# Performance work log

Hardware: AMD Instinct MI355X
Metric: run time of the kernel (lower is better)

## Reference

```python
import jax, jax.numpy as jnp
import numpy as np
import math

EMBED_DIM = 1024
NUM_HEADS = 16
DEPTH = 12
HEAD_DIM = EMBED_DIM // NUM_HEADS // 2  # 32
LAMBDA_INIT = 0.8 - 0.6 * math.exp(-0.3 * DEPTH)
SCALE = HEAD_DIM ** -0.5  # flash_attn default softmax scale
RMS_EPS = 1e-5
BATCH, SEQ = 2, 2048


def _freqs(seq_len):
    # angle = 1 / 10000 ** linspace(0, 1, head_dim//2); freqs = pos * angle
    angle = 1.0 / 10000.0 ** jnp.linspace(0.0, 1.0, HEAD_DIM // 2)
    idx = jnp.arange(seq_len, dtype=jnp.float32)
    f = idx[:, None] * angle[None, :]
    return jnp.cos(f), jnp.sin(f)


def _rope_interleaved(x, cos, sin):
    # x: (b, t, h, d); cos/sin: (t, d//2). Interleaved pairs (0,1),(2,3),...
    x1, x2 = x[..., 0::2], x[..., 1::2]
    c = cos[None, :, None, :]
    s = sin[None, :, None, :]
    o1 = x1 * c - x2 * s
    o2 = x1 * s + x2 * c
    return jnp.stack([o1, o2], axis=-1).reshape(x.shape)


def _forward(x, Wq, Wk, Wv, Wo, lambda_q1, lambda_k1, lambda_q2, lambda_k2, rms_weight):
    b, t, _ = x.shape
    q = (x @ Wq.T).reshape(b, t, 2 * NUM_HEADS, HEAD_DIM)
    k = (x @ Wk.T).reshape(b, t, 2 * NUM_HEADS, HEAD_DIM)
    v = (x @ Wv.T).reshape(b, t, NUM_HEADS, 2, HEAD_DIM)
    cos, sin = _freqs(t)
    q = _rope_interleaved(q, cos, sin)
    k = _rope_interleaved(k, cos, sin)
    # split the 2H axis into (H, 2): q1/q2 are even/odd sub-heads
    q = q.reshape(b, t, NUM_HEADS, 2, HEAD_DIM)
    k = k.reshape(b, t, NUM_HEADS, 2, HEAD_DIM)
    q1, q2 = q[..., 0, :], q[..., 1, :]
    k1, k2 = k[..., 0, :], k[..., 1, :]
    v12 = v.reshape(b, t, NUM_HEADS, 2 * HEAD_DIM)  # == concat(v1, v2) on last dim

    def attend(qh, kh):
        scores = jnp.einsum('bthd,bshd->bhts', qh, kh) * SCALE
        p = jax.nn.softmax(scores, axis=-1)  # non-causal, as in source
        return jnp.einsum('bhts,bshe->bthe', p, v12)  # (b, t, H, 2*hd)

    attn1 = attend(q1, k1)
    attn2 = attend(q2, k2)
    lam = (jnp.exp(jnp.sum(lambda_q1 * lambda_k1))
           - jnp.exp(jnp.sum(lambda_q2 * lambda_k2)) + LAMBDA_INIT)
    a = attn1 - lam * attn2
    # RMSNorm over last dim (2*head_dim) with affine weight
    a = a * jax.lax.rsqrt(jnp.mean(a * a, axis=-1, keepdims=True) + RMS_EPS) * rms_weight
    a = a * (1.0 - LAMBDA_INIT)
    a = a.reshape(b, t, NUM_HEADS * 2 * HEAD_DIM)
    return a @ Wo.T


def setup_inputs() -> dict:
    key = jax.random.key(0)
    ks = jax.random.split(key, 9)
    std = EMBED_DIM ** -0.5
    return {
        'x': jax.random.normal(ks[0], (BATCH, SEQ, EMBED_DIM), jnp.float32),
        'Wq': jax.random.normal(ks[1], (EMBED_DIM, EMBED_DIM), jnp.float32) * std,
        'Wk': jax.random.normal(ks[2], (EMBED_DIM, EMBED_DIM), jnp.float32) * std,
        'Wv': jax.random.normal(ks[3], (EMBED_DIM, EMBED_DIM), jnp.float32) * std,
        'Wo': jax.random.normal(ks[4], (EMBED_DIM, EMBED_DIM), jnp.float32) * std,
        'lambda_q1': jax.random.normal(ks[5], (HEAD_DIM,), jnp.float32) * 0.1,
        'lambda_k1': jax.random.normal(ks[6], (HEAD_DIM,), jnp.float32) * 0.1,
        'lambda_q2': jax.random.normal(ks[7], (HEAD_DIM,), jnp.float32) * 0.1,
        'lambda_k2': jax.random.normal(ks[8], (HEAD_DIM,), jnp.float32) * 0.1,
        'rms_weight': jnp.ones((2 * HEAD_DIM,), jnp.float32),
    }


def reference(x, Wq, Wk, Wv, Wo, lambda_q1, lambda_k1, lambda_q2, lambda_k2, rms_weight):
    return _forward(x, Wq, Wk, Wv, Wo, lambda_q1, lambda_k1, lambda_q2, lambda_k2, rms_weight)
```

## Files before the change

kernel.cpp:

```cpp
#include <hip/hip_runtime.h>
#include <stdint.h>

typedef unsigned short u16;
typedef __bf16 bf16x8 __attribute__((ext_vector_type(8)));
typedef float f32x4 __attribute__((ext_vector_type(4)));
typedef float f32x16 __attribute__((ext_vector_type(16)));

#define TOKENS 4096
#define SEQLEN 2048
#define EMB 1024
#define NHEADS 16

static constexpr float LAMBDA_INIT_F = 0.7836057665316245f;
static constexpr float ONE_MINUS_LI  = 0.21639423346837553f;
static constexpr float SCALE_F       = 0.17677669529663687f;
static constexpr float LOG2E_F       = 1.4426950408889634f;

__device__ __forceinline__ u16 f2bf(float f) {
  uint32_t u = __builtin_bit_cast(uint32_t, f);
  u += 0x7fffu + ((u >> 16) & 1u);
  return (u16)(u >> 16);
}
__device__ __forceinline__ float bf2f(u16 h) {
  uint32_t u = ((uint32_t)h) << 16;
  return __builtin_bit_cast(float, u);
}
__device__ __forceinline__ float fast_exp2(float x) {
#if __has_builtin(__builtin_amdgcn_exp2f)
  return __builtin_amdgcn_exp2f(x);
#else
  return exp2f(x);
#endif
}
__device__ __forceinline__ void async16(const void* g, void* l) {
  __builtin_amdgcn_global_load_lds((__attribute__((address_space(1))) void*)(g),
                                   (__attribute__((address_space(3))) void*)(l),
                                   16, 0, 0);
}
__device__ __forceinline__ f32x4 mfma16(uint4 a, uint4 b, f32x4 c) {
  return __builtin_amdgcn_mfma_f32_16x16x32_bf16(
      __builtin_bit_cast(bf16x8, a), __builtin_bit_cast(bf16x8, b), c, 0, 0, 0);
}
__device__ __forceinline__ f32x16 mfma32(uint4 a, uint4 b, f32x16 c) {
  return __builtin_amdgcn_mfma_f32_32x32x16_bf16(
      __builtin_bit_cast(bf16x8, a), __builtin_bit_cast(bf16x8, b), c, 0, 0, 0);
}

__global__ __launch_bounds__(256) void prep_kernel(
    const float* __restrict__ x,  const float* __restrict__ wq,
    const float* __restrict__ wk, const float* __restrict__ wv,
    const float* __restrict__ wo, const float* __restrict__ lq1,
    const float* __restrict__ lk1,const float* __restrict__ lq2,
    const float* __restrict__ lk2,
    u16* __restrict__ xb, u16* __restrict__ wqb, u16* __restrict__ wkb,
    u16* __restrict__ wvb, u16* __restrict__ wob, float* __restrict__ lam_out)
{
  int i0 = (blockIdx.x * 256 + threadIdx.x) * 4;
  const float* src; u16* dst; int j;
  if (i0 < 4194304)      { src = x;  dst = xb;  j = i0; }
  else if (i0 < 5242880) { src = wq; dst = wqb; j = i0 - 4194304; }
  else if (i0 < 6291456) { src = wk; dst = wkb; j = i0 - 5242880; }
  else if (i0 < 7340032) { src = wv; dst = wvb; j = i0 - 6291456; }
  else                   { src = wo; dst = wob; j = i0 - 7340032; }
  float4 v = *(const float4*)(src + j);
  uint2 pack;
  pack.x = (uint32_t)f2bf(v.x) | ((uint32_t)f2bf(v.y) << 16);
  pack.y = (uint32_t)f2bf(v.z) | ((uint32_t)f2bf(v.w) << 16);
  *(uint2*)(dst + j) = pack;

  if (blockIdx.x == 0 && threadIdx.x == 0) {
    float d1 = 0.f, d2 = 0.f;
    for (int i = 0; i < 32; ++i) { d1 += lq1[i] * lk1[i]; d2 += lq2[i] * lk2[i]; }
    *lam_out = expf(d1) - expf(d2) + LAMBDA_INIT_F;
  }
}

template <int MODE>
__device__ __forceinline__ void gemm_body(const u16* __restrict__ A,
                                          const u16* __restrict__ B,
                                          void* __restrict__ C)
{
  __shared__ u16 As[128 * 64];
  __shared__ u16 Bs[128 * 64];
  const int t = threadIdx.x;
  const int lane = t & 63, w = t >> 6;
  const int q4 = lane >> 4, lm = lane & 15;
  const int wr = w >> 1, wc = w & 1;
  const int bm = blockIdx.y * 128, bn = blockIdx.x * 128;

  f32x4 acc[4][4];
#pragma unroll
  for (int mi = 0; mi < 4; ++mi)
#pragma unroll
    for (int ni = 0; ni < 4; ++ni) acc[mi][ni] = (f32x4){0.f, 0.f, 0.f, 0.f};

  for (int kt = 0; kt < 16; ++kt) {
    const int k0 = kt * 64;
    __syncthreads();
#pragma unroll
    for (int ro = 0; ro < 4; ++ro) {
      int ft = ro * 256 + t;
      int row = ft >> 3;
      int col = (((ft & 7) ^ (row & 7)) << 3);
      async16(&A[(bm + row) * 1024 + k0 + col], &As[ft * 8]);
      async16(&B[(bn + row) * 1024 + k0 + col], &Bs[ft * 8]);
    }
    __syncthreads();
#pragma unroll
    for (int ks = 0; ks < 2; ++ks) {
      uint4 af[4], bf[4];
#pragma unroll
      for (int mi = 0; mi < 4; ++mi)
        af[mi] = *(const uint4*)&As[(wr * 64 + mi * 16 + lm) * 64 +
                                    (((ks * 4 + q4) ^ (lm & 7)) << 3)];
#pragma unroll
      for (int ni = 0; ni < 4; ++ni)
        bf[ni] = *(const uint4*)&Bs[(wc * 64 + ni * 16 + lm) * 64 +
                                    (((ks * 4 + q4) ^ (lm & 7)) << 3)];
#pragma unroll
      for (int mi = 0; mi < 4; ++mi)
#pragma unroll
        for (int ni = 0; ni < 4; ++ni)
          acc[mi][ni] = mfma16(af[mi], bf[ni], acc[mi][ni]);
    }
  }
#pragma unroll
  for (int mi = 0; mi < 4; ++mi)
#pragma unroll
    for (int ni = 0; ni < 4; ++ni) {
      if (MODE == 2) {
        int token0 = bm + wr * 64 + mi * 16 + q4 * 4;
        int col = bn + wc * 64 + ni * 16 + lm;
        int bb = token0 >> 11, key0 = token0 & 2047;
        int h = col >> 6, d = col & 63;
        ushort4 pk;
        pk.x = f2bf(acc[mi][ni][0]);
        pk.y = f2bf(acc[mi][ni][1]);
        pk.z = f2bf(acc[mi][ni][2]);
        pk.w = f2bf(acc[mi][ni][3]);
        *(ushort4*)((u16*)C + ((size_t)((bb * 16 + h) * 64 + d)) * 2048 + key0) = pk;
      } else {
#pragma unroll
        for (int r = 0; r < 4; ++r) {
          int row = bm + wr * 64 + mi * 16 + q4 * 4 + r;
          int col = bn + wc * 64 + ni * 16 + lm;
          if (MODE == 1) ((float*)C)[row * 1024 + col] = acc[mi][ni][r];
          else           ((u16*)C)[row * 1024 + col]   = f2bf(acc[mi][ni][r]);
        }
      }
    }
}

__global__ __launch_bounds__(256) void gemm_qkv_kernel(
    const u16* __restrict__ xb, const u16* __restrict__ wqb,
    const u16* __restrict__ wkb, const u16* __restrict__ wvb,
    u16* __restrict__ qb, u16* __restrict__ kb, u16* __restrict__ vtb)
{
  if (blockIdx.z == 0)      gemm_body<0>(xb, wqb, qb);
  else if (blockIdx.z == 1) gemm_body<0>(xb, wkb, kb);
  else                      gemm_body<2>(xb, wvb, vtb);
}

__global__ __launch_bounds__(256) void gemm_out_kernel(
    const u16* __restrict__ ab, const u16* __restrict__ wob,
    float* __restrict__ out)
{
  gemm_body<1>(ab, wob, out);
}

__global__ __launch_bounds__(256) void rope_kernel(u16* __restrict__ qb,
                                                   u16* __restrict__ kb)
{
  int p = blockIdx.x * 256 + threadIdx.x;
  int tok = p >> 9;
  int pc = p & 511;
  int j = pc & 15;
  int tpos = tok & (SEQLEN - 1);
  float ang = exp2f(-(float)j * 0.8858474919699633f);
  float f = (float)tpos * ang;
  float s, c;
  sincosf(f, &s, &c);
  u16* ptr = ((blockIdx.y == 0) ? qb : kb) + tok * 1024 + pc * 2;
  uint32_t u = *(const uint32_t*)ptr;
  float x1 = bf2f((u16)(u & 0xffff));
  float x2 = bf2f((u16)(u >> 16));
  float o1 = x1 * c - x2 * s;
  float o2 = x1 * s + x2 * c;
  if (blockIdx.y == 0) { o1 *= SCALE_F * LOG2E_F; o2 *= SCALE_F * LOG2E_F; }
  *(uint32_t*)ptr = (uint32_t)f2bf(o1) | ((uint32_t)f2bf(o2) << 16);
}

__global__ __launch_bounds__(256) void attn_kernel(
    const u16* __restrict__ qb, const u16* __restrict__ kb,
    const u16* __restrict__ vtb, const float* __restrict__ lam_p,
    const float* __restrict__ rmsw, u16* __restrict__ ab)
{
  __shared__ u16 smem[16384];

  const int t = threadIdx.x;
  const int lane = t & 63, w = t >> 6;
  const int l5 = lane >> 5, lr = lane & 31;
  const int qt = blockIdx.x, h = blockIdx.y, b = blockIdx.z;
  const int tok0 = b * SEQLEN + qt * 128;
  const int hch = h * 64;

  const u16* kbase = kb + (size_t)(b * SEQLEN) * 1024 + hch;
  const u16* vbase = vtb + (size_t)((b * 16 + h) * 64) * 2048;
  u16* P = &smem[8192 + w * 2048];

#pragma unroll
  for (int ro = 0; ro < 4; ++ro) {
    int ft = ro * 256 + t;
    int row = ft >> 3;
    int col = (((ft & 7) ^ (row & 7)) << 3);
    async16(&qb[(tok0 + row) * 1024 + hch + col], &smem[8192 + ft * 8]);
  }
  __syncthreads();
  uint4 qf[2][2];
#pragma unroll
  for (int c = 0; c < 2; ++c)
#pragma unroll
    for (int kk = 0; kk < 2; ++kk)
      qf[c][kk] = *(const uint4*)&smem[8192 + (w * 32 + lr) * 64 +
                                       (((c * 4 + kk * 2 + l5) ^ (lr & 7)) << 3)];

  f32x16 O[2][2];
#pragma unroll
  for (int c = 0; c < 2; ++c)
#pragma unroll
    for (int n = 0; n < 2; ++n)
#pragma unroll
      for (int i = 0; i < 16; ++i) O[c][n][i] = 0.f;
  float rs[2] = {0.f, 0.f};
  uint4 vf[2][4];

  for (int kv = 0; kv < SEQLEN; kv += 64) {
    __syncthreads();
#pragma unroll
    for (int ro = 0; ro < 2; ++ro) {
      int ft = ro * 256 + t;
      int row = ft >> 3;
      int col = (((ft & 7) ^ (row & 7)) << 3);
      async16(kbase + (kv + row) * 1024 + col, &smem[ft * 8]);
      async16(vbase + row * 2048 + kv + col, &smem[4096 + ft * 8]);
    }
    __syncthreads();

#pragma unroll
    for (int c = 0; c < 2; ++c) {
#pragma unroll
      for (int kb2 = 0; kb2 < 2; ++kb2) {
        f32x16 s;
#pragma unroll
        for (int i = 0; i < 16; ++i) s[i] = 0.f;
#pragma unroll
        for (int kk = 0; kk < 2; ++kk) {
          uint4 kf = *(const uint4*)&smem[(kb2 * 32 + lr) * 64 +
                                          (((c * 4 + kk * 2 + l5) ^ (lr & 7)) << 3)];
          s = mfma32(kf, qf[c][kk], s);
        }
        float rloc = 0.f;
#pragma unroll
        for (int g = 0; g < 4; ++g) {
          float e0 = fast_exp2(s[g * 4 + 0]);
          float e1 = fast_exp2(s[g * 4 + 1]);
          float e2 = fast_exp2(s[g * 4 + 2]);
          float e3 = fast_exp2(s[g * 4 + 3]);
          rloc += (e0 + e1) + (e2 + e3);
          uint2 pk;
          pk.x = __builtin_amdgcn_perm(__builtin_bit_cast(uint32_t, e1),
                                       __builtin_bit_cast(uint32_t, e0), 0x07060302u);
          pk.y = __builtin_amdgcn_perm(__builtin_bit_cast(uint32_t, e3),
                                       __builtin_bit_cast(uint32_t, e2), 0x07060302u);
          *(uint2*)&P[lr * 64 + ((((kb2 * 4 + g) ^ (lr & 7)) << 3) + l5 * 4)] = pk;
        }
        rs[c] += rloc;
      }
      if (c == 0) {
#pragma unroll
        for (int n = 0; n < 2; ++n)
#pragma unroll
          for (int kc = 0; kc < 4; ++kc)
            vf[n][kc] = *(const uint4*)&smem[4096 + (n * 32 + lr) * 64 +
                                             (((kc * 2 + l5) ^ (lr & 7)) << 3)];
      }
#pragma unroll
      for (int kc = 0; kc < 4; ++kc) {
        uint4 af = *(const uint4*)&P[lr * 64 + (((kc * 2 + l5) ^ (lr & 7)) << 3)];
        O[c][0] = mfma32(af, vf[0][kc], O[c][0]);
        O[c][1] = mfma32(af, vf[1][kc], O[c][1]);
      }
    }
  }

  float lam = *lam_p;
  rs[0] += __shfl_xor(rs[0], 32);
  rs[1] += __shfl_xor(rs[1], 32);
  float inv1 = 1.f / rs[0];
  float inv2 = lam / rs[1];
  float wv2[2] = { rmsw[lr], rmsw[32 + lr] };
#pragma unroll
  for (int g = 0; g < 4; ++g) {
#pragma unroll
    for (int rr = 0; rr < 4; ++rr) {
      int r = g * 4 + rr;
      int qrl = rr + 8 * g + 4 * l5;
      float i1 = __shfl(inv1, qrl);
      float i2 = __shfl(inv2, qrl);
      float a0 = O[0][0][r] * i1 - O[1][0][r] * i2;
      float a1 = O[0][1][r] * i1 - O[1][1][r] * i2;
      float ssq = a0 * a0 + a1 * a1;
#pragma unroll
      for (int off = 16; off > 0; off >>= 1) ssq += __shfl_xor(ssq, off);
      float sc = rsqrtf(ssq * (1.f / 64.f) + 1e-5f) * ONE_MINUS_LI;
      int row = tok0 + w * 32 + qrl;
      ab[row * 1024 + hch + lr]      = f2bf(a0 * sc * wv2[0]);
      ab[row * 1024 + hch + 32 + lr] = f2bf(a1 * sc * wv2[1]);
    }
  }
}

extern "C" void kernel_launch(void* const* d_in, const int* in_sizes, int n_in,
                              void* d_out, int out_size, void* d_ws, size_t ws_size,
                              hipStream_t stream)
{
  (void)in_sizes; (void)n_in; (void)out_size; (void)ws_size;
  const float* x    = (const float*)d_in[0];
  const float* Wq   = (const float*)d_in[1];
  const float* Wk   = (const float*)d_in[2];
  const float* Wv   = (const float*)d_in[3];
  const float* Wo   = (const float*)d_in[4];
  const float* lq1  = (const float*)d_in[5];
  const float* lk1  = (const float*)d_in[6];
  const float* lq2  = (const float*)d_in[7];
  const float* lk2  = (const float*)d_in[8];
  const float* rmsw = (const float*)d_in[9];
  float* out = (float*)d_out;

  char* ws = (char*)d_ws;
  u16* xb   = (u16*)(ws + 0);
  u16* wqb  = (u16*)(ws + 8388608);
  u16* wkb  = (u16*)(ws + 10485760);
  u16* wvb  = (u16*)(ws + 12582912);
  u16* wob  = (u16*)(ws + 14680064);
  u16* qb   = (u16*)(ws + 16777216);
  u16* kb   = (u16*)(ws + 25165824);
  u16* vtb  = (u16*)(ws + 33554432);
  u16* ab   = (u16*)(ws + 41943040);
  float* lam = (float*)(ws + 50331648);

  hipLaunchKernelGGL(prep_kernel, dim3(8192), dim3(256), 0, stream,
                     x, Wq, Wk, Wv, Wo, lq1, lk1, lq2, lk2,
                     xb, wqb, wkb, wvb, wob, lam);
  hipLaunchKernelGGL(gemm_qkv_kernel, dim3(8, 32, 3), dim3(256), 0, stream,
                     xb, wqb, wkb, wvb, qb, kb, vtb);
  hipLaunchKernelGGL(rope_kernel, dim3(8192, 2), dim3(256), 0, stream, qb, kb);
  hipLaunchKernelGGL(attn_kernel, dim3(16, 16, 2), dim3(256), 0, stream,
                     qb, kb, vtb, lam, rmsw, ab);
  hipLaunchKernelGGL(gemm_out_kernel, dim3(8, 32, 1), dim3(256), 0, stream,
                     ab, wob, out);
}
```

Measured before the change: 252.8 us.

## Split attention sub-heads across waves and keep P in registers via lane shuffles

The attention kernel now uses 64-query tiles and twice as many blocks. Each wave handles one sub-head (c) for one 32-row group, instead of one wave handling both sub-heads for 32 rows. The P matrix is no longer round-tripped through shared memory: the S^T layout is computed and swapped between half-waves with shuffles to form the MFMA B operand directly. The differential combine now goes through shared memory between wave pairs. Shared memory is halved and launch bounds request 4 blocks per CU, which aims for better occupancy and less LDS traffic, at the cost of extra K/V tile loads per query and an extra sync and exchange in the epilogue.

```diff
diff --git a/kernel.cpp b/kernel.cpp
--- a/kernel.cpp
+++ b/kernel.cpp
@@ -190,49 +190,45 @@
   *(uint32_t*)ptr = (uint32_t)f2bf(o1) | ((uint32_t)f2bf(o2) << 16);
 }
 
-__global__ __launch_bounds__(256) void attn_kernel(
+__global__ __launch_bounds__(256, 4) void attn_kernel(
     const u16* __restrict__ qb, const u16* __restrict__ kb,
     const u16* __restrict__ vtb, const float* __restrict__ lam_p,
     const float* __restrict__ rmsw, u16* __restrict__ ab)
 {
-  __shared__ u16 smem[16384];
+  __shared__ u16 smem[8192];
 
   const int t = threadIdx.x;
   const int lane = t & 63, w = t >> 6;
   const int l5 = lane >> 5, lr = lane & 31;
+  const int c = w >> 1, rg = w & 1;
+  const bool hi = (l5 != 0);
   const int qt = blockIdx.x, h = blockIdx.y, b = blockIdx.z;
-  const int tok0 = b * SEQLEN + qt * 128;
+  const int tok0 = b * SEQLEN + qt * 64;
   const int hch = h * 64;
 
   const u16* kbase = kb + (size_t)(b * SEQLEN) * 1024 + hch;
   const u16* vbase = vtb + (size_t)((b * 16 + h) * 64) * 2048;
-  u16* P = &smem[8192 + w * 2048];
-
-#pragma unroll
-  for (int ro = 0; ro < 4; ++ro) {
+
+#pragma unroll
+  for (int ro = 0; ro < 2; ++ro) {
     int ft = ro * 256 + t;
     int row = ft >> 3;
     int col = (((ft & 7) ^ (row & 7)) << 3);
-    async16(&qb[(tok0 + row) * 1024 + hch + col], &smem[8192 + ft * 8]);
+    async16(&qb[(tok0 + row) * 1024 + hch + col], &smem[ft * 8]);
   }
   __syncthreads();
-  uint4 qf[2][2];
-#pragma unroll
-  for (int c = 0; c < 2; ++c)
-#pragma unroll
-    for (int kk = 0; kk < 2; ++kk)
-      qf[c][kk] = *(const uint4*)&smem[8192 + (w * 32 + lr) * 64 +
-                                       (((c * 4 + kk * 2 + l5) ^ (lr & 7)) << 3)];
-
-  f32x16 O[2][2];
-#pragma unroll
-  for (int c = 0; c < 2; ++c)
-#pragma unroll
-    for (int n = 0; n < 2; ++n)
-#pragma unroll
-      for (int i = 0; i < 16; ++i) O[c][n][i] = 0.f;
-  float rs[2] = {0.f, 0.f};
-  uint4 vf[2][4];
+  uint4 qf[2];
+#pragma unroll
+  for (int kk = 0; kk < 2; ++kk)
+    qf[kk] = *(const uint4*)&smem[(rg * 32 + lr) * 64 +
+                                  (((c * 4 + kk * 2 + l5) ^ (lr & 7)) << 3)];
+
+  f32x16 O[2];
+#pragma unroll
+  for (int db = 0; db < 2; ++db)
+#pragma unroll
+    for (int i = 0; i < 16; ++i) O[db][i] = 0.f;
+  float rs = 0.f;
 
   for (int kv = 0; kv < SEQLEN; kv += 64) {
     __syncthreads();
@@ -246,77 +242,117 @@
     }
     __syncthreads();
 
-#pragma unroll
-    for (int c = 0; c < 2; ++c) {
-#pragma unroll
-      for (int kb2 = 0; kb2 < 2; ++kb2) {
-        f32x16 s;
-#pragma unroll
-        for (int i = 0; i < 16; ++i) s[i] = 0.f;
-#pragma unroll
-        for (int kk = 0; kk < 2; ++kk) {
-          uint4 kf = *(const uint4*)&smem[(kb2 * 32 + lr) * 64 +
-                                          (((c * 4 + kk * 2 + l5) ^ (lr & 7)) << 3)];
-          s = mfma32(kf, qf[c][kk], s);
-        }
-        float rloc = 0.f;
-#pragma unroll
-        for (int g = 0; g < 4; ++g) {
-          float e0 = fast_exp2(s[g * 4 + 0]);
-          float e1 = fast_exp2(s[g * 4 + 1]);
-          float e2 = fast_exp2(s[g * 4 + 2]);
-          float e3 = fast_exp2(s[g * 4 + 3]);
-          rloc += (e0 + e1) + (e2 + e3);
-          uint2 pk;
-          pk.x = __builtin_amdgcn_perm(__builtin_bit_cast(uint32_t, e1),
-                                       __builtin_bit_cast(uint32_t, e0), 0x07060302u);
-          pk.y = __builtin_amdgcn_perm(__builtin_bit_cast(uint32_t, e3),
-                                       __builtin_bit_cast(uint32_t, e2), 0x07060302u);
-          *(uint2*)&P[lr * 64 + ((((kb2 * 4 + g) ^ (lr & 7)) << 3) + l5 * 4)] = pk;
-        }
-        rs[c] += rloc;
-      }
-      if (c == 0) {
-#pragma unroll
-        for (int n = 0; n < 2; ++n)
-#pragma unroll
-          for (int kc = 0; kc < 4; ++kc)
-            vf[n][kc] = *(const uint4*)&smem[4096 + (n * 32 + lr) * 64 +
-                                             (((kc * 2 + l5) ^ (lr & 7)) << 3)];
-      }
-#pragma unroll
-      for (int kc = 0; kc < 4; ++kc) {
-        uint4 af = *(const uint4*)&P[lr * 64 + (((kc * 2 + l5) ^ (lr & 7)) << 3)];
-        O[c][0] = mfma32(af, vf[0][kc], O[c][0]);
-        O[c][1] = mfma32(af, vf[1][kc], O[c][1]);
-      }
-    }
-  }
-
-  float lam = *lam_p;
-  rs[0] += __shfl_xor(rs[0], 32);
-  rs[1] += __shfl_xor(rs[1], 32);
-  float inv1 = 1.f / rs[0];
-  float inv2 = lam / rs[1];
-  float wv2[2] = { rmsw[lr], rmsw[32 + lr] };
-#pragma unroll
-  for (int g = 0; g < 4; ++g) {
-#pragma unroll
-    for (int rr = 0; rr < 4; ++rr) {
-      int r = g * 4 + rr;
-      int qrl = rr + 8 * g + 4 * l5;
-      float i1 = __shfl(inv1, qrl);
-      float i2 = __shfl(inv2, qrl);
-      float a0 = O[0][0][r] * i1 - O[1][0][r] * i2;
-      float a1 = O[0][1][r] * i1 - O[1][1][r] * i2;
-      float ssq = a0 * a0 + a1 * a1;
-#pragma unroll
-      for (int off = 16; off > 0; off >>= 1) ssq += __shfl_xor(ssq, off);
-      float sc = rsqrtf(ssq * (1.f / 64.f) + 1e-5f) * ONE_MINUS_LI;
-      int row = tok0 + w * 32 + qrl;
-      ab[row * 1024 + hch + lr]      = f2bf(a0 * sc * wv2[0]);
-      ab[row * 1024 + hch + 32 + lr] = f2bf(a1 * sc * wv2[1]);
-    }
+    uint4 vf[2][4];
+#pragma unroll
+    for (int db = 0; db < 2; ++db)
+#pragma unroll
+      for (int kc = 0; kc < 4; ++kc)
+        vf[db][kc] = *(const uint4*)&smem[4096 + (db * 32 + lr) * 64 +
+                                          (((kc * 2 + l5) ^ (lr & 7)) << 3)];
+
+#pragma unroll
+    for (int kb2 = 0; kb2 < 2; ++kb2) {
+      f32x16 s;
+#pragma unroll
+      for (int i = 0; i < 16; ++i) s[i] = 0.f;
+#pragma unroll
+      for (int kk = 0; kk < 2; ++kk) {
+        uint4 kf = *(const uint4*)&smem[(kb2 * 32 + lr) * 64 +
+                                        (((c * 4 + kk * 2 + l5) ^ (lr & 7)) << 3)];
+        s = mfma32(kf, qf[kk], s);
+      }
+      uint32_t pk[8];
+      float rloc = 0.f;
+#pragma unroll
+      for (int g = 0; g < 4; ++g) {
+        float e0 = fast_exp2(s[g * 4 + 0]);
+        float e1 = fast_exp2(s[g * 4 + 1]);
+        float e2 = fast_exp2(s[g * 4 + 2]);
+        float e3 = fast_exp2(s[g * 4 + 3]);
+        rloc += (e0 + e1) + (e2 + e3);
+        pk[2 * g]     = __builtin_amdgcn_perm(__builtin_bit_cast(uint32_t, e1),
+                                              __builtin_bit_cast(uint32_t, e0),
+                                              0x07060302u);
+        pk[2 * g + 1] = __builtin_amdgcn_perm(__builtin_bit_cast(uint32_t, e3),
+                                              __builtin_bit_cast(uint32_t, e2),
+                                              0x07060302u);
+      }
+      rs += rloc;
+#pragma unroll
+      for (int t2 = 0; t2 < 2; ++t2) {
+        uint32_t s0 = hi ? pk[4 * t2]     : pk[4 * t2 + 2];
+        uint32_t s1 = hi ? pk[4 * t2 + 1] : pk[4 * t2 + 3];
+        uint32_t r0 = (uint32_t)__shfl_xor((int)s0, 32);
+        uint32_t r1 = (uint32_t)__shfl_xor((int)s1, 32);
+        uint4 bfr;
+        bfr.x = hi ? r0 : pk[4 * t2];
+        bfr.y = hi ? r1 : pk[4 * t2 + 1];
+        bfr.z = hi ? pk[4 * t2 + 2] : r0;
+        bfr.w = hi ? pk[4 * t2 + 3] : r1;
+        O[0] = mfma32(vf[0][kb2 * 2 + t2], bfr, O[0]);
+        O[1] = mfma32(vf[1][kb2 * 2 + t2], bfr, O[1]);
+      }
+    }
+  }
+
+  rs += __shfl_xor(rs, 32);
+  const int row64 = rg * 32 + lr;
+  float* ex = (float*)smem;
+  __syncthreads();
+
+  if (c == 1) {
+    float inv2 = (*lam_p) / rs;
+#pragma unroll
+    for (int db = 0; db < 2; ++db)
+#pragma unroll
+      for (int g = 0; g < 4; ++g) {
+        int d0 = db * 32 + 8 * g + 4 * l5;
+        int ch = (d0 >> 2) ^ (lr & 7);
+        float4 v;
+        v.x = O[db][4 * g + 0] * inv2;
+        v.y = O[db][4 * g + 1] * inv2;
+        v.z = O[db][4 * g + 2] * inv2;
+        v.w = O[db][4 * g + 3] * inv2;
+        *(float4*)&ex[row64 * 64 + ch * 4] = v;
+      }
+  }
+  __syncthreads();
+  if (c == 0) {
+    float inv1 = 1.f / rs;
+    float4 a4[8];
+    float ssq = 0.f;
+#pragma unroll
+    for (int db = 0; db < 2; ++db)
+#pragma unroll
+      for (int g = 0; g < 4; ++g) {
+        int d0 = db * 32 + 8 * g + 4 * l5;
+        int ch = (d0 >> 2) ^ (lr & 7);
+        float4 o2 = *(const float4*)&ex[row64 * 64 + ch * 4];
+        float4 v;
+        v.x = O[db][4 * g + 0] * inv1 - o2.x;
+        v.y = O[db][4 * g + 1] * inv1 - o2.y;
+        v.z = O[db][4 * g + 2] * inv1 - o2.z;
+        v.w = O[db][4 * g + 3] * inv1 - o2.w;
+        ssq += v.x * v.x + v.y * v.y + v.z * v.z + v.w * v.w;
+        a4[db * 4 + g] = v;
+      }
+    ssq += __shfl_xor(ssq, 32);
+    float sc = rsqrtf(ssq * (1.f / 64.f) + 1e-5f) * ONE_MINUS_LI;
+    const int rowg = tok0 + row64;
+#pragma unroll
+    for (int db = 0; db < 2; ++db)
+#pragma unroll
+      for (int g = 0; g < 4; ++g) {
+        int d0 = db * 32 + 8 * g + 4 * l5;
+        float4 wv = *(const float4*)&rmsw[d0];
+        float4 v = a4[db * 4 + g];
+        ushort4 pq;
+        pq.x = f2bf(v.x * sc * wv.x);
+        pq.y = f2bf(v.y * sc * wv.y);
+        pq.z = f2bf(v.z * sc * wv.z);
+        pq.w = f2bf(v.w * sc * wv.w);
+        *(ushort4*)&ab[rowg * 1024 + hch + d0] = pq;
+      }
   }
 }
 
@@ -355,7 +391,7 @@
   hipLaunchKernelGGL(gemm_qkv_kernel, dim3(8, 32, 3), dim3(256), 0, stream,
                      xb, wqb, wkb, wvb, qb, kb, vtb);
   hipLaunchKernelGGL(rope_kernel, dim3(8192, 2), dim3(256), 0, stream, qb, kb);
-  hipLaunchKernelGGL(attn_kernel, dim3(16, 16, 2), dim3(256), 0, stream,
+  hipLaunchKernelGGL(attn_kernel, dim3(32, 16, 2), dim3(256), 0, stream,
                      qb, kb, vtb, lam, rmsw, ab);
   hipLaunchKernelGGL(gemm_out_kernel, dim3(8, 32, 1), dim3(256), 0, stream,
                      ab, wob, out);
```

Result: faster. 240.1 us (-5.0%).
